# Optimization experiments

Hardware: AMD Instinct MI355X
Metric: run time of the kernel (lower is better)

The kernel has to match this reference:

```python
import jax, jax.numpy as jnp
import numpy as np

D_MODEL, D_K, D_V, H = 512, 64, 64, 8
B, NQ, NK = 4, 2048, 2048


def setup_inputs() -> dict:
    key = jax.random.key(0)
    ks = jax.random.split(key, 14)
    s = 0.02
    return {
        "queries": jax.random.normal(ks[0], (B, NQ, D_MODEL), jnp.float32),
        "keys": jax.random.normal(ks[1], (B, NK, D_MODEL), jnp.float32),
        "values": jax.random.normal(ks[2], (B, NK, D_MODEL), jnp.float32),
        "attention_weights": jax.random.uniform(ks[3], (B, H, NQ, NK), jnp.float32),
        "attention_mask": jax.random.bernoulli(ks[4], 0.1, (B, H, NQ, NK)),
        "Wq": jax.random.normal(ks[5], (D_MODEL, H * D_K), jnp.float32) * s,
        "bq": jnp.zeros((H * D_K,), jnp.float32),
        "Wk": jax.random.normal(ks[6], (D_MODEL, H * D_K), jnp.float32) * s,
        "bk": jnp.zeros((H * D_K,), jnp.float32),
        "Wv": jax.random.normal(ks[7], (D_MODEL, H * D_V), jnp.float32) * s,
        "bv": jnp.zeros((H * D_V,), jnp.float32),
        "Wo": jax.random.normal(ks[8], (H * D_V, D_MODEL), jnp.float32) * s,
        "bo": jnp.zeros((D_MODEL,), jnp.float32),
    }


def reference(queries, keys, values, attention_weights, attention_mask,
              Wq, bq, Wk, bk, Wv, bv, Wo, bo):
    b_s, nq, _ = queries.shape
    nk = keys.shape[1]
    # projections -> (b, h, seq, d)
    q = (queries @ Wq + bq).reshape(b_s, nq, H, D_K).transpose(0, 2, 1, 3)
    k = (keys @ Wk + bk).reshape(b_s, nk, H, D_K).transpose(0, 2, 1, 3)
    v = (values @ Wv + bv).reshape(b_s, nk, H, D_V).transpose(0, 2, 1, 3)
    scale = 1.0 / np.sqrt(D_K).astype(np.float32)
    att = jnp.einsum("bhqd,bhkd->bhqk", q, k) * scale
    att = att * attention_weights
    att = jnp.where(attention_mask, -jnp.inf, att)
    att = jax.nn.softmax(att, axis=-1)
    out = jnp.einsum("bhqk,bhkd->bhqd", att, v)
    out = out.transpose(0, 2, 1, 3).reshape(b_s, nq, H * D_V)
    return out @ Wo + bo
```

## Files before the change

kernel.cpp:

```cpp
#include <hip/hip_runtime.h>
#include <hip/hip_bf16.h>
#include <math.h>

#define B_   4
#define H_   8
#define NQ_  2048
#define NK_  2048
#define DM_  512
#define DK_  64
#define WL_  262144

typedef short  bf16x8 __attribute__((ext_vector_type(8)));
typedef float  f32x4  __attribute__((ext_vector_type(4)));

static __device__ __forceinline__ f32x4 MFMA16(bf16x8 a, bf16x8 b, f32x4 c) {
    return __builtin_amdgcn_mfma_f32_16x16x32_bf16(a, b, c, 0, 0, 0);
}
static __device__ __forceinline__ unsigned short f2bf(float f) {
    __hip_bfloat16 h = __float2bfloat16(f);
    unsigned short u; __builtin_memcpy(&u, &h, 2); return u;
}
static __device__ __forceinline__ float bf2f(unsigned short u) {
    unsigned int x = ((unsigned int)u) << 16;
    float f; __builtin_memcpy(&f, &x, 4); return f;
}
static __device__ __forceinline__ void glds16(const void* g, void* l) {
    __builtin_amdgcn_global_load_lds(
        (__attribute__((address_space(1))) const void*)g,
        (__attribute__((address_space(3))) void*)l, 16, 0, 0);
}

__global__ __launch_bounds__(256) void wprep(const float* __restrict__ Wq,
                                             const float* __restrict__ Wk,
                                             const float* __restrict__ Wv,
                                             const float* __restrict__ Wo,
                                             unsigned short* __restrict__ out)
{
    __shared__ float tile[64][65];
    const int tid = threadIdx.x;
    const int k0 = blockIdx.x * 64, n0 = blockIdx.y * 64, w = blockIdx.z;
    const float* W = (w == 0) ? Wq : (w == 1) ? Wk : (w == 2) ? Wv : Wo;
    unsigned short* WTh = out + (size_t)w * 2 * WL_;
    unsigned short* WTl = WTh + WL_;

#pragma unroll
    for (int rd = 0; rd < 4; ++rd) {
        const int k = (tid >> 4) + 16*rd, c4 = (tid & 15) * 4;
        const float4 v4 = *(const float4*)(W + (size_t)(k0 + k)*DM_ + n0 + c4);
        tile[k][c4+0] = v4.x; tile[k][c4+1] = v4.y;
        tile[k][c4+2] = v4.z; tile[k][c4+3] = v4.w;
    }
    __syncthreads();
#pragma unroll
    for (int rd = 0; rd < 4; ++rd) {
        const int n = (tid >> 4) + 16*rd, kk = (tid & 15) * 4;
        unsigned short hh[4], ll[4];
#pragma unroll
        for (int j = 0; j < 4; ++j) {
            const float f = tile[kk + j][n];
            hh[j] = f2bf(f);
            ll[j] = f2bf(f - bf2f(hh[j]));
        }
        *(ushort4*)(WTh + (size_t)(n0 + n)*DM_ + k0 + kk) = make_ushort4(hh[0],hh[1],hh[2],hh[3]);
        *(ushort4*)(WTl + (size_t)(n0 + n)*DM_ + k0 + kk) = make_ushort4(ll[0],ll[1],ll[2],ll[3]);
    }
}

__global__ __launch_bounds__(256) void proj_mask(
    const float* __restrict__ q, const float* __restrict__ k,
    const float* __restrict__ v,
    const unsigned short* __restrict__ wt,
    const float* __restrict__ bq, const float* __restrict__ bk,
    const float* __restrict__ bv,
    unsigned short* __restrict__ q_bf, unsigned short* __restrict__ k_bf,
    unsigned short* __restrict__ vT,
    const unsigned char* __restrict__ Mk,
    unsigned long long* __restrict__ bits)
{
    __shared__ unsigned short Ah[64][64], Bh[64][64], Bl[64][64];
    __shared__ int s_flag;

    const int tid = threadIdx.x;
    const int z = blockIdx.z;

    if (z < 3) {
        const float* A = (z == 0) ? q : (z == 1) ? k : v;
        const unsigned short* WTh = wt + (size_t)(2*z) * WL_;
        const unsigned short* WTl = WTh + WL_;
        const float* bias = (z == 0) ? bq : (z == 1) ? bk : bv;
        const float oscale = (z == 0) ? 0.125f : 1.0f;
        const int mode = (z == 2) ? 1 : 0;

        const int w = tid >> 6, lane = tid & 63, g = lane >> 4, r = lane & 15;
        const int m0 = blockIdx.x * 64, n0 = blockIdx.y * 64;

        char* pAh = (char*)&Ah[0][0];
        char* pBh = (char*)&Bh[0][0];
        char* pBl = (char*)&Bl[0][0];

        const f32x4 z4 = {0.f, 0.f, 0.f, 0.f};
        f32x4 acc[4] = {z4, z4, z4, z4};

        for (int kt = 0; kt < DM_; kt += 64) {
#pragma unroll
            for (int rd = 0; rd < 4; ++rd) {
                const int row = (tid >> 4) + 16*rd;
                const int c4  = (tid & 15) * 4;
                const float4 a4 = *(const float4*)(A + (size_t)(m0 + row)*DM_ + kt + c4);
                const float av[4] = {a4.x, a4.y, a4.z, a4.w};
                unsigned short hh[4];
#pragma unroll
                for (int j = 0; j < 4; ++j) hh[j] = f2bf(av[j]);
                const int bo = (c4 * 2) ^ ((row & 7) << 4);
                *(ushort4*)(pAh + row*128 + bo) = make_ushort4(hh[0],hh[1],hh[2],hh[3]);
            }
#pragma unroll
            for (int rd = 0; rd < 2; ++rd) {
                const int idx = tid + 256*rd;
                const int row = idx >> 3;
                const int cb  = (idx & 7) * 16;
                const int bo  = cb ^ ((row & 7) << 4);
                const size_t goff = (size_t)(n0 + row)*DM_ + kt + (cb >> 1);
                *(bf16x8*)(pBh + row*128 + bo) = *(const bf16x8*)(WTh + goff);
                *(bf16x8*)(pBl + row*128 + bo) = *(const bf16x8*)(WTl + goff);
            }
            __syncthreads();

            const int swr = (r & 7) << 4;
#pragma unroll
            for (int ks = 0; ks < 2; ++ks) {
                const int xo = (64*ks + 16*g) ^ swr;
                const bf16x8 xh = *(const bf16x8*)(pAh + (16*w + r)*128 + xo);
#pragma unroll
                for (int nt = 0; nt < 4; ++nt) {
                    const bf16x8 bh = *(const bf16x8*)(pBh + (16*nt + r)*128 + xo);
                    const bf16x8 bl = *(const bf16x8*)(pBl + (16*nt + r)*128 + xo);
                    if (mode == 1) {
                        acc[nt] = MFMA16(xh, bh, acc[nt]);
                        acc[nt] = MFMA16(xh, bl, acc[nt]);
                    } else {
                        acc[nt] = MFMA16(bh, xh, acc[nt]);
                        acc[nt] = MFMA16(bl, xh, acc[nt]);
                    }
                }
            }
            __syncthreads();
        }

        if (mode == 0) {
            const int m = m0 + 16*w + r;
            const int b = m >> 11, qq = m & 2047, h = blockIdx.y;
            unsigned short* dstp = (z == 0 ? q_bf : k_bf) +
                                   (((size_t)(b*H_ + h))*NQ_ + qq)*DK_;
#pragma unroll
            for (int nt = 0; nt < 4; ++nt) {
                unsigned short u[4];
#pragma unroll
                for (int j = 0; j < 4; ++j)
                    u[j] = f2bf((acc[nt][j] + bias[n0 + 16*nt + 4*g + j]) * oscale);
                *(ushort4*)(dstp + 16*nt + 4*g) = make_ushort4(u[0],u[1],u[2],u[3]);
            }
        } else {
            const int b = m0 >> 11, h = blockIdx.y;
            const int key = (m0 & 2047) + 16*w + 4*g;
#pragma unroll
            for (int nt = 0; nt < 4; ++nt) {
                const int dv = 16*nt + r;
                const float bvv = bias[n0 + dv];
                unsigned short u[4];
#pragma unroll
                for (int j = 0; j < 4; ++j) u[j] = f2bf(acc[nt][j] + bvv);
                *(ushort4*)(vT + (((size_t)(b*H_ + h))*DK_ + dv)*NK_ + key) =
                    make_ushort4(u[0],u[1],u[2],u[3]);
            }
        }
    } else {
        if (tid == 0) s_flag = 0;
        __syncthreads();
        {
            bool any = false;
#pragma unroll
            for (int i = 1; i < 16; i += 4)
                if (Mk[tid*16 + i]) any = true;
            if (any) s_flag = 1;
        }
        __syncthreads();

        const long long NELEM = (long long)B_*H_*NQ_*NK_;
        const long long nblk  = 2LL * gridDim.x * gridDim.y;
        const long long nth   = nblk * 256;
        const long long id    = ((long long)(z - 3) * gridDim.x * gridDim.y +
                                 (long long)blockIdx.y * gridDim.x + blockIdx.x);
        const long long T     = id * 256 + tid;
        unsigned short* b16   = (unsigned short*)bits;
        const uint4*    src   = (const uint4*)Mk;

        if (s_flag) {
            const long long n = NELEM / 16;
            for (long long t = T; t < n; t += nth) {
                const uint4 u = src[t];
                const unsigned int w[4] = {u.x, u.y, u.z, u.w};
                unsigned int m = 0;
#pragma unroll
                for (int j = 0; j < 4; ++j)
#pragma unroll
                    for (int b2 = 0; b2 < 4; ++b2)
                        if ((w[j] >> (8*b2)) & 0xffu) m |= 1u << (4*j + b2);
                b16[t] = (unsigned short)m;
            }
        } else {
            const long long n = NELEM / 4;
            const int l3 = tid & 3;
            for (long long t = T; t < n; t += nth) {
                const uint4 u = src[t];
                const unsigned int nib = (u.x ? 1u : 0u) | (u.y ? 2u : 0u) |
                                         (u.z ? 4u : 0u) | (u.w ? 8u : 0u);
                unsigned int vv = nib << (4*l3);
                vv |= __shfl_xor(vv, 1, 64);
                vv |= __shfl_xor(vv, 2, 64);
                if (l3 == 0) b16[t >> 2] = (unsigned short)vv;
            }
        }
    }
}

template<int MODE>
__global__ __launch_bounds__(256) void gemm_split(
    const float* __restrict__ A,
    const unsigned short* __restrict__ WTh,
    const unsigned short* __restrict__ WTl,
    const float* __restrict__ bias,
    void* __restrict__ outv, const float oscale)
{
    __shared__ unsigned short Ah[64][64], Al[64][64], Bh[64][64], Bl[64][64];

    const int tid = threadIdx.x;
    const int w = tid >> 6, lane = tid & 63, g = lane >> 4, r = lane & 15;
    const int m0 = blockIdx.x * 64, n0 = blockIdx.y * 64;

    char* pAh = (char*)&Ah[0][0];
    char* pAl = (char*)&Al[0][0];
    char* pBh = (char*)&Bh[0][0];
    char* pBl = (char*)&Bl[0][0];

    const f32x4 z4 = {0.f, 0.f, 0.f, 0.f};
    f32x4 acc[4] = {z4, z4, z4, z4};

    for (int kt = 0; kt < DM_; kt += 64) {
#pragma unroll
        for (int rd = 0; rd < 4; ++rd) {
            const int row = (tid >> 4) + 16*rd;
            const int c4  = (tid & 15) * 4;
            const float4 a4 = *(const float4*)(A + (size_t)(m0 + row)*DM_ + kt + c4);
            const float av[4] = {a4.x, a4.y, a4.z, a4.w};
            unsigned short hh[4];
#pragma unroll
            for (int j = 0; j < 4; ++j) hh[j] = f2bf(av[j]);
            const int bo = (c4 * 2) ^ ((row & 7) << 4);
            *(ushort4*)(pAh + row*128 + bo) = make_ushort4(hh[0],hh[1],hh[2],hh[3]);
            if (MODE == 2) {
                unsigned short ll[4];
#pragma unroll
                for (int j = 0; j < 4; ++j) ll[j] = f2bf(av[j] - bf2f(hh[j]));
                *(ushort4*)(pAl + row*128 + bo) = make_ushort4(ll[0],ll[1],ll[2],ll[3]);
            }
        }
#pragma unroll
        for (int rd = 0; rd < 2; ++rd) {
            const int idx = tid + 256*rd;
            const int row = idx >> 3;
            const int cb  = (idx & 7) * 16;
            const int bo  = cb ^ ((row & 7) << 4);
            const size_t goff = (size_t)(n0 + row)*DM_ + kt + (cb >> 1);
            *(bf16x8*)(pBh + row*128 + bo) = *(const bf16x8*)(WTh + goff);
            *(bf16x8*)(pBl + row*128 + bo) = *(const bf16x8*)(WTl + goff);
        }
        __syncthreads();

        const int swr = (r & 7) << 4;
#pragma unroll
        for (int ks = 0; ks < 2; ++ks) {
            const int xo = (64*ks + 16*g) ^ swr;
            const bf16x8 xh = *(const bf16x8*)(pAh + (16*w + r)*128 + xo);
#pragma unroll
            for (int nt = 0; nt < 4; ++nt) {
                const bf16x8 bh = *(const bf16x8*)(pBh + (16*nt + r)*128 + xo);
                const bf16x8 bl = *(const bf16x8*)(pBl + (16*nt + r)*128 + xo);
                const bf16x8 xl = *(const bf16x8*)(pAl + (16*w + r)*128 + xo);
                acc[nt] = MFMA16(bh, xh, acc[nt]);
                acc[nt] = MFMA16(bh, xl, acc[nt]);
                acc[nt] = MFMA16(bl, xh, acc[nt]);
            }
        }
        __syncthreads();
    }

    {
        const int m = m0 + 16*w + r;
        float* dst = (float*)outv + (size_t)m*DM_ + n0;
#pragma unroll
        for (int nt = 0; nt < 4; ++nt) {
            float4 o4;
            o4.x = acc[nt][0] + bias[n0 + 16*nt + 4*g + 0];
            o4.y = acc[nt][1] + bias[n0 + 16*nt + 4*g + 1];
            o4.z = acc[nt][2] + bias[n0 + 16*nt + 4*g + 2];
            o4.w = acc[nt][3] + bias[n0 + 16*nt + 4*g + 3];
            *(float4*)(dst + 16*nt + 4*g) = o4;
        }
    }
    (void)oscale;
}

__global__ __launch_bounds__(256, 4) void attn_mfma(
    const unsigned short* __restrict__ Qb,
    const unsigned short* __restrict__ Kb,
    const unsigned short* __restrict__ Vt,
    const float* __restrict__ Wt,
    const unsigned long long* __restrict__ Mb,
    float* __restrict__ O)
{
    __shared__ unsigned short KT[64][64];
    __shared__ unsigned short VTs[64][64];
    __shared__ float          WT[64][64];
    __shared__ short          Pl[4][1024];

    const int tid  = threadIdx.x;
    const int wv   = tid >> 6, lane = tid & 63;
    const int g    = lane >> 4, r = lane & 15;

    const int l    = blockIdx.x;
    const int xcd  = l & 7, t = l >> 3;
    const int bh   = ((t >> 5) << 3) + xcd;
    const int qblk = t & 31;
    const int q0   = qblk * 64 + wv * 16;

    const size_t kvBase = (size_t)bh * NK_ * DK_;
    const unsigned short* qp = Qb + kvBase + (size_t)(q0 + r)*DK_ + 8*g;
    const bf16x8 qf0 = *(const bf16x8*)qp;
    const bf16x8 qf1 = *(const bf16x8*)(qp + 32);

    const float* wblock = Wt + ((size_t)bh*NQ_ + qblk*64)*NK_;
    const unsigned long long* brow = Mb + ((size_t)bh*NQ_ + q0 + r)*(NK_/64);
    const unsigned short* kg = Kb + kvBase;
    const unsigned short* vg = Vt + kvBase;

    const f32x4 zero4 = {0.f, 0.f, 0.f, 0.f};
    f32x4 oa0 = zero4, oa1 = zero4, oa2 = zero4, oa3 = zero4;
    float m_run = -1e30f, l_run = 0.f;

    char* pbase = (char*)&Pl[wv][0];
    const int roff = r * 128;
    const int sw   = (r & 7) << 4;

    const int kv_soff = 8 * ((lane & 7) ^ (lane >> 3));
    const int kv_r8   = lane >> 3;
    const int w_r4    = lane >> 4;

#pragma unroll 1
    for (int i = 0; i < 32; ++i) {
        const int kt = i * 64;

#pragma unroll
        for (int c = 0; c < 2; ++c) {
            const int rowl = 16*wv + c*8 + kv_r8;
            glds16(kg + (size_t)(kt + rowl)*DK_ + kv_soff,
                   &KT[16*wv + c*8][0] + lane*8);
            glds16(vg + (size_t)rowl*NK_ + kt + kv_soff,
                   &VTs[16*wv + c*8][0] + lane*8);
        }
#pragma unroll
        for (int c = 0; c < 4; ++c) {
            const int rowl = 16*wv + c*4 + w_r4;
            glds16(wblock + (size_t)rowl*NK_ + kt + 4*((lane & 15) ^ (c*4 + w_r4)),
                   &WT[16*wv + c*4][0] + lane*4);
        }
        const unsigned long long bcur = brow[i];
        __syncthreads();

        f32x4 sa0 = zero4, sa1 = zero4, sa2 = zero4, sa3 = zero4;
        {
            const bf16x8 k00 = *(const bf16x8*)&KT[ 0 + r][8*((g    ) ^ (r & 7))];
            const bf16x8 k01 = *(const bf16x8*)&KT[ 0 + r][8*((g + 4) ^ (r & 7))];
            const bf16x8 k10 = *(const bf16x8*)&KT[16 + r][8*((g    ) ^ (r & 7))];
            const bf16x8 k11 = *(const bf16x8*)&KT[16 + r][8*((g + 4) ^ (r & 7))];
            const bf16x8 k20 = *(const bf16x8*)&KT[32 + r][8*((g    ) ^ (r & 7))];
            const bf16x8 k21 = *(const bf16x8*)&KT[32 + r][8*((g + 4) ^ (r & 7))];
            const bf16x8 k30 = *(const bf16x8*)&KT[48 + r][8*((g    ) ^ (r & 7))];
            const bf16x8 k31 = *(const bf16x8*)&KT[48 + r][8*((g + 4) ^ (r & 7))];
            sa0 = MFMA16(k00, qf0, sa0); sa0 = MFMA16(k01, qf1, sa0);
            sa1 = MFMA16(k10, qf0, sa1); sa1 = MFMA16(k11, qf1, sa1);
            sa2 = MFMA16(k20, qf0, sa2); sa2 = MFMA16(k21, qf1, sa2);
            sa3 = MFMA16(k30, qf0, sa3); sa3 = MFMA16(k31, qf1, sa3);
        }

        f32x4 wf[4];
#pragma unroll
        for (int t2 = 0; t2 < 4; ++t2)
            wf[t2] = *(const f32x4*)&WT[16*wv + r][4*((4*t2 + g) ^ r)];

        float lg[16];
        const f32x4 sav[4] = {sa0, sa1, sa2, sa3};
#pragma unroll
        for (int t2 = 0; t2 < 4; ++t2) {
            const unsigned int half = (t2 & 2) ? (unsigned int)(bcur >> 32)
                                               : (unsigned int)bcur;
#pragma unroll
            for (int j = 0; j < 4; ++j) {
                const unsigned int bit = (half >> (16*(t2 & 1) + 4*g + j)) & 1u;
                lg[4*t2+j] = bit ? -1e30f : sav[t2][j] * wf[t2][j];
            }
        }

        float mx = lg[0];
#pragma unroll
        for (int i2 = 1; i2 < 16; ++i2) mx = fmaxf(mx, lg[i2]);
        mx = fmaxf(mx, __shfl_xor(mx, 16, 64));
        mx = fmaxf(mx, __shfl_xor(mx, 32, 64));
        const float mnew = fmaxf(m_run, mx);
        const float fsc  = __expf(m_run - mnew);
        m_run = mnew;
        float p16[16], rs = 0.f;
#pragma unroll
        for (int i2 = 0; i2 < 16; ++i2) { p16[i2] = __expf(lg[i2] - mnew); rs += p16[i2]; }
        rs += __shfl_xor(rs, 16, 64);
        rs += __shfl_xor(rs, 32, 64);
        l_run = l_run * fsc + rs;

#pragma unroll
        for (int t2 = 0; t2 < 4; ++t2) {
            const unsigned int w0 = (unsigned int)f2bf(p16[4*t2+0]) |
                                    ((unsigned int)f2bf(p16[4*t2+1]) << 16);
            const unsigned int w1 = (unsigned int)f2bf(p16[4*t2+2]) |
                                    ((unsigned int)f2bf(p16[4*t2+3]) << 16);
            *(int2*)(pbase + roff + ((32*t2 + 8*g) ^ sw)) = make_int2((int)w0, (int)w1);
        }
        const bf16x8 pa0 = *(const bf16x8*)(pbase + roff + ((     16*g) ^ sw));
        const bf16x8 pa1 = *(const bf16x8*)(pbase + roff + ((64 + 16*g) ^ sw));

        float fr[4];
#pragma unroll
        for (int j = 0; j < 4; ++j) fr[j] = __shfl(fsc, 4*g + j, 64);
#pragma unroll
        for (int j = 0; j < 4; ++j) {
            oa0[j] *= fr[j]; oa1[j] *= fr[j]; oa2[j] *= fr[j]; oa3[j] *= fr[j];
        }

        {
            const bf16x8 v00 = *(const bf16x8*)&VTs[ 0 + r][8*((g    ) ^ (r & 7))];
            const bf16x8 v01 = *(const bf16x8*)&VTs[16 + r][8*((g    ) ^ (r & 7))];
            const bf16x8 v02 = *(const bf16x8*)&VTs[32 + r][8*((g    ) ^ (r & 7))];
            const bf16x8 v03 = *(const bf16x8*)&VTs[48 + r][8*((g    ) ^ (r & 7))];
            const bf16x8 v10 = *(const bf16x8*)&VTs[ 0 + r][8*((g + 4) ^ (r & 7))];
            const bf16x8 v11 = *(const bf16x8*)&VTs[16 + r][8*((g + 4) ^ (r & 7))];
            const bf16x8 v12 = *(const bf16x8*)&VTs[32 + r][8*((g + 4) ^ (r & 7))];
            const bf16x8 v13 = *(const bf16x8*)&VTs[48 + r][8*((g + 4) ^ (r & 7))];
            oa0 = MFMA16(pa0, v00, oa0); oa1 = MFMA16(pa0, v01, oa1);
            oa2 = MFMA16(pa0, v02, oa2); oa3 = MFMA16(pa0, v03, oa3);
            oa0 = MFMA16(pa1, v10, oa0); oa1 = MFMA16(pa1, v11, oa1);
            oa2 = MFMA16(pa1, v12, oa2); oa3 = MFMA16(pa1, v13, oa3);
        }
        __syncthreads();
    }

    const float inv = 1.0f / l_run;
    float ir[4];
#pragma unroll
    for (int j = 0; j < 4; ++j) ir[j] = __shfl(inv, 4*g + j, 64);
    const int bb = bh >> 3, h = bh & 7;
    const f32x4 oav[4] = {oa0, oa1, oa2, oa3};
#pragma unroll
    for (int nt = 0; nt < 4; ++nt)
#pragma unroll
        for (int j = 0; j < 4; ++j)
            O[((size_t)(bb*NQ_ + q0 + 4*g + j))*DM_ + h*64 + 16*nt + r] = oav[nt][j] * ir[j];
}

extern "C" void kernel_launch(void* const* d_in, const int* in_sizes, int n_in,
                              void* d_out, int out_size, void* d_ws, size_t ws_size,
                              hipStream_t stream) {
    (void)in_sizes; (void)n_in; (void)out_size; (void)ws_size;

    const float* q    = (const float*)d_in[0];
    const float* k    = (const float*)d_in[1];
    const float* v    = (const float*)d_in[2];
    const float* attw = (const float*)d_in[3];
    const unsigned char* mask = (const unsigned char*)d_in[4];
    const float* Wq = (const float*)d_in[5];
    const float* bq = (const float*)d_in[6];
    const float* Wk = (const float*)d_in[7];
    const float* bk = (const float*)d_in[8];
    const float* Wv = (const float*)d_in[9];
    const float* bv = (const float*)d_in[10];
    const float* Wo = (const float*)d_in[11];
    const float* bo = (const float*)d_in[12];
    float* out = (float*)d_out;

    const long long NE = (long long)B_*H_*NQ_*DK_;
    unsigned short* q_bf = (unsigned short*)d_ws;
    unsigned short* k_bf = q_bf + NE;
    unsigned short* vT   = q_bf + 2*NE;
    unsigned short* wt   = q_bf + 3*NE;
    unsigned long long* bits = (unsigned long long*)(wt + 8LL*WL_);
    const long long NB = (long long)B_*H_*NQ_*NK_/64;
    float* o_ws = (float*)(bits + NB);

    const dim3 blk(256);
    wprep<<<dim3(8, 8, 4), blk, 0, stream>>>(Wq, Wk, Wv, Wo, wt);

    proj_mask<<<dim3(128, 8, 5), blk, 0, stream>>>(q, k, v, wt, bq, bk, bv,
                                                   q_bf, k_bf, vT, mask, bits);

    attn_mfma<<<dim3(1024), blk, 0, stream>>>(q_bf, k_bf, vT, attw, bits, o_ws);

    gemm_split<2><<<dim3(128, 8), blk, 0, stream>>>(o_ws, wt + 6*WL_, wt + 7*WL_, bo, out, 1.0f);
}
```

Baseline: 340.7 us.

## Load K/V fragments directly from global and double-buffer weight tile in LDS

Drops LDS staging for K and V: each wave now loads its MFMA fragments straight from global memory (L2-cached, shared across the four waves). The attention-weight tile becomes double-buffered in LDS, so the next tile is prefetched while the current one is consumed, leaving one barrier per iteration. This frees LDS and the mid-iteration barrier, but each wave now re-reads K/V from global/L2, which adds load latency and traffic.

```diff
diff --git a/kernel.cpp b/kernel.cpp
--- a/kernel.cpp
+++ b/kernel.cpp
@@ -319,10 +319,8 @@
     const unsigned long long* __restrict__ Mb,
     float* __restrict__ O)
 {
-    __shared__ unsigned short KT[64][64];
-    __shared__ unsigned short VTs[64][64];
-    __shared__ float          WT[64][64];
-    __shared__ short          Pl[4][1024];
+    __shared__ float WT[2][64][64];
+    __shared__ short Pl[4][1024];
 
     const int tid  = threadIdx.x;
     const int wv   = tid >> 6, lane = tid & 63;
@@ -341,8 +339,8 @@
 
     const float* wblock = Wt + ((size_t)bh*NQ_ + qblk*64)*NK_;
     const unsigned long long* brow = Mb + ((size_t)bh*NQ_ + q0 + r)*(NK_/64);
-    const unsigned short* kg = Kb + kvBase;
-    const unsigned short* vg = Vt + kvBase;
+    const unsigned short* kbase = Kb + kvBase + (size_t)r*DK_ + 8*g;
+    const unsigned short* vbase = Vt + kvBase + (size_t)r*NK_ + 8*g;
 
     const f32x4 zero4 = {0.f, 0.f, 0.f, 0.f};
     f32x4 oa0 = zero4, oa1 = zero4, oa2 = zero4, oa3 = zero4;
@@ -351,52 +349,58 @@
     char* pbase = (char*)&Pl[wv][0];
     const int roff = r * 128;
     const int sw   = (r & 7) << 4;
-
-    const int kv_soff = 8 * ((lane & 7) ^ (lane >> 3));
-    const int kv_r8   = lane >> 3;
-    const int w_r4    = lane >> 4;
-
-#pragma unroll 1
-    for (int i = 0; i < 32; ++i) {
-        const int kt = i * 64;
-
-#pragma unroll
-        for (int c = 0; c < 2; ++c) {
-            const int rowl = 16*wv + c*8 + kv_r8;
-            glds16(kg + (size_t)(kt + rowl)*DK_ + kv_soff,
-                   &KT[16*wv + c*8][0] + lane*8);
-            glds16(vg + (size_t)rowl*NK_ + kt + kv_soff,
-                   &VTs[16*wv + c*8][0] + lane*8);
-        }
+    const int w_r4 = lane >> 4;
+
+    auto stageW = [&](int pbuf, int kt) {
 #pragma unroll
         for (int c = 0; c < 4; ++c) {
             const int rowl = 16*wv + c*4 + w_r4;
             glds16(wblock + (size_t)rowl*NK_ + kt + 4*((lane & 15) ^ (c*4 + w_r4)),
-                   &WT[16*wv + c*4][0] + lane*4);
-        }
+                   &WT[pbuf][16*wv + c*4][0] + lane*4);
+        }
+    };
+
+#define LOADK(ktv) do { \
+    const unsigned short* kp_ = kbase + (size_t)(ktv)*DK_;      \
+    k00 = *(const bf16x8*)kp_;         k01 = *(const bf16x8*)(kp_ + 32);          \
+    k10 = *(const bf16x8*)(kp_+1024);  k11 = *(const bf16x8*)(kp_ + 1024 + 32);   \
+    k20 = *(const bf16x8*)(kp_+2048);  k21 = *(const bf16x8*)(kp_ + 2048 + 32);   \
+    k30 = *(const bf16x8*)(kp_+3072);  k31 = *(const bf16x8*)(kp_ + 3072 + 32);   \
+} while (0)
+
+#define LOADV(ktv) do { \
+    const unsigned short* vp_ = vbase + (ktv);                  \
+    v00 = *(const bf16x8*)(vp_);             v01 = *(const bf16x8*)(vp_ + 16*NK_);      \
+    v02 = *(const bf16x8*)(vp_ + 32*NK_);    v03 = *(const bf16x8*)(vp_ + 48*NK_);      \
+    v10 = *(const bf16x8*)(vp_ + 32);        v11 = *(const bf16x8*)(vp_ + 16*NK_ + 32); \
+    v12 = *(const bf16x8*)(vp_ + 32*NK_+32); v13 = *(const bf16x8*)(vp_ + 48*NK_ + 32); \
+} while (0)
+
+    bf16x8 k00,k01,k10,k11,k20,k21,k30,k31;
+    bf16x8 v00,v01,v02,v03, v10,v11,v12,v13;
+
+    stageW(0, 0);
+    __syncthreads();
+
+#pragma unroll 1
+    for (int i = 0; i < 32; ++i) {
+        const int p  = i & 1;
+        const int kt = i * 64;
+
+        LOADK(kt);
+        if (i + 1 < 32) stageW(p ^ 1, kt + 64);
         const unsigned long long bcur = brow[i];
-        __syncthreads();
 
         f32x4 sa0 = zero4, sa1 = zero4, sa2 = zero4, sa3 = zero4;
-        {
-            const bf16x8 k00 = *(const bf16x8*)&KT[ 0 + r][8*((g    ) ^ (r & 7))];
-            const bf16x8 k01 = *(const bf16x8*)&KT[ 0 + r][8*((g + 4) ^ (r & 7))];
-            const bf16x8 k10 = *(const bf16x8*)&KT[16 + r][8*((g    ) ^ (r & 7))];
-            const bf16x8 k11 = *(const bf16x8*)&KT[16 + r][8*((g + 4) ^ (r & 7))];
-            const bf16x8 k20 = *(const bf16x8*)&KT[32 + r][8*((g    ) ^ (r & 7))];
-            const bf16x8 k21 = *(const bf16x8*)&KT[32 + r][8*((g + 4) ^ (r & 7))];
-            const bf16x8 k30 = *(const bf16x8*)&KT[48 + r][8*((g    ) ^ (r & 7))];
-            const bf16x8 k31 = *(const bf16x8*)&KT[48 + r][8*((g + 4) ^ (r & 7))];
-            sa0 = MFMA16(k00, qf0, sa0); sa0 = MFMA16(k01, qf1, sa0);
-            sa1 = MFMA16(k10, qf0, sa1); sa1 = MFMA16(k11, qf1, sa1);
-            sa2 = MFMA16(k20, qf0, sa2); sa2 = MFMA16(k21, qf1, sa2);
-            sa3 = MFMA16(k30, qf0, sa3); sa3 = MFMA16(k31, qf1, sa3);
-        }
+        sa0 = MFMA16(k00, qf0, sa0); sa0 = MFMA16(k01, qf1, sa0);
+        sa1 = MFMA16(k10, qf0, sa1); sa1 = MFMA16(k11, qf1, sa1);
+        sa2 = MFMA16(k20, qf0, sa2); sa2 = MFMA16(k21, qf1, sa2);
+        sa3 = MFMA16(k30, qf0, sa3); sa3 = MFMA16(k31, qf1, sa3);
 
         f32x4 wf[4];
 #pragma unroll
         for (int t2 = 0; t2 < 4; ++t2)
-            wf[t2] = *(const f32x4*)&WT[16*wv + r][4*((4*t2 + g) ^ r)];
+            wf[t2] = *(const f32x4*)&WT[p][16*wv + r][4*((4*t2 + g) ^ r)];
 
         float lg[16];
         const f32x4 sav[4] = {sa0, sa1, sa2, sa3};
@@ -437,6 +441,8 @@
         const bf16x8 pa0 = *(const bf16x8*)(pbase + roff + ((     16*g) ^ sw));
         const bf16x8 pa1 = *(const bf16x8*)(pbase + roff + ((64 + 16*g) ^ sw));
 
+        LOADV(kt);
+
         float fr[4];
 #pragma unroll
         for (int j = 0; j < 4; ++j) fr[j] = __shfl(fsc, 4*g + j, 64);
@@ -445,22 +451,15 @@
             oa0[j] *= fr[j]; oa1[j] *= fr[j]; oa2[j] *= fr[j]; oa3[j] *= fr[j];
         }
 
-        {
-            const bf16x8 v00 = *(const bf16x8*)&VTs[ 0 + r][8*((g    ) ^ (r & 7))];
-            const bf16x8 v01 = *(const bf16x8*)&VTs[16 + r][8*((g    ) ^ (r & 7))];
-            const bf16x8 v02 = *(const bf16x8*)&VTs[32 + r][8*((g    ) ^ (r & 7))];
-            const bf16x8 v03 = *(const bf16x8*)&VTs[48 + r][8*((g    ) ^ (r & 7))];
-            const bf16x8 v10 = *(const bf16x8*)&VTs[ 0 + r][8*((g + 4) ^ (r & 7))];
-            const bf16x8 v11 = *(const bf16x8*)&VTs[16 + r][8*((g + 4) ^ (r & 7))];
-            const bf16x8 v12 = *(const bf16x8*)&VTs[32 + r][8*((g + 4) ^ (r & 7))];
-            const bf16x8 v13 = *(const bf16x8*)&VTs[48 + r][8*((g + 4) ^ (r & 7))];
-            oa0 = MFMA16(pa0, v00, oa0); oa1 = MFMA16(pa0, v01, oa1);
-            oa2 = MFMA16(pa0, v02, oa2); oa3 = MFMA16(pa0, v03, oa3);
-            oa0 = MFMA16(pa1, v10, oa0); oa1 = MFMA16(pa1, v11, oa1);
-            oa2 = MFMA16(pa1, v12, oa2); oa3 = MFMA16(pa1, v13, oa3);
-        }
+        oa0 = MFMA16(pa0, v00, oa0); oa1 = MFMA16(pa0, v01, oa1);
+        oa2 = MFMA16(pa0, v02, oa2); oa3 = MFMA16(pa0, v03, oa3);
+        oa0 = MFMA16(pa1, v10, oa0); oa1 = MFMA16(pa1, v11, oa1);
+        oa2 = MFMA16(pa1, v12, oa2); oa3 = MFMA16(pa1, v13, oa3);
+
         __syncthreads();
     }
+#undef LOADK
+#undef LOADV
 
     const float inv = 1.0f / l_run;
     float ir[4];
```

Result: slower. 483.1 us (+41.8%).
